# Kernel optimization log

Measured on AMD Instinct MI355X. Metric: run time of the kernel, lower is better.

Reference implementation:

```python
import jax, jax.numpy as jnp
import numpy as np

N_NODES = 50000
N_EDGES = 800000
D = 128


def setup_inputs() -> dict:
    key = jax.random.key(0)
    ks = jax.random.split(key, 8)
    x = jax.random.normal(ks[0], (N_NODES, D), dtype=jnp.float32)
    src = jax.random.randint(ks[1], (N_EDGES,), 0, N_NODES, dtype=jnp.int64)
    dst = jax.random.randint(ks[2], (N_EDGES,), 0, N_NODES, dtype=jnp.int64)
    edge_weights = jax.random.uniform(ks[3], (N_EDGES,), dtype=jnp.float32)
    scale = 1.0 / np.sqrt(D)
    W1 = jax.random.normal(ks[4], (D, D), dtype=jnp.float32) * scale
    b1 = jnp.zeros((D,), dtype=jnp.float32)
    W2 = jax.random.normal(ks[5], (D, D), dtype=jnp.float32) * scale
    b2 = jnp.zeros((D,), dtype=jnp.float32)
    return {"x": x, "src": src, "dst": dst, "edge_weights": edge_weights,
            "W1": W1, "b1": b1, "W2": W2, "b2": b2}


def reference(x, src, dst, edge_weights, W1, b1, W2, b2):
    n_nodes = x.shape[0]
    # out-degrees (edges where node is the source), clamped to >= 1
    deg = jax.ops.segment_sum(jnp.ones_like(src, dtype=x.dtype), src,
                              num_segments=n_nodes)
    deg = jnp.maximum(deg, 1.0)
    # per-edge symmetric-normalization coefficient: 1/sqrt(deg_u * deg_v)
    coef = jax.lax.rsqrt(deg[src] * deg[dst]) * edge_weights  # [E]
    # gather-multiply-scatter: sum_{u->v} x[u] * coef into node v
    msgs = x[src] * coef[:, None]                              # [E, D]
    agg = jax.ops.segment_sum(msgs, dst, num_segments=n_nodes)  # [N, D]
    # FFN: Linear -> ReLU -> Linear (dropout = 0)
    h = jax.nn.relu(agg @ W1 + b1)
    return h @ W2 + b2
```

## Files before the change

kernel.cpp:

```cpp
#include <hip/hip_runtime.h>

#define NN 50000
#define NE 800000
#define D  128
#define HB 128
#define CH 6272
#define PW 50176
#define XB 128
#define RB2 98
#define GRANGE 12544

typedef short short8 __attribute__((ext_vector_type(8)));
typedef float f32x4  __attribute__((ext_vector_type(4)));
typedef unsigned char u8;

__device__ __forceinline__ ushort f2bf(float f) {
    union { float f; unsigned u; } v; v.f = f;
    unsigned r = v.u + 0x7FFFu + ((v.u >> 16) & 1u);
    return (ushort)(r >> 16);
}


__global__ __launch_bounds__(1024) void prep_kernel(const int* __restrict__ src,
                                                    const int* __restrict__ dst,
                                                    const float* __restrict__ x,
                                                    const float* __restrict__ W1,
                                                    const float* __restrict__ W2,
                                                    u8* __restrict__ psrc,
                                                    u8* __restrict__ pdst,
                                                    ushort* __restrict__ xbf,
                                                    ushort* __restrict__ W1t,
                                                    ushort* __restrict__ W2t) {
    __shared__ unsigned bins[2 * PW / 4];
    const int t = threadIdx.x, b = blockIdx.x;

    if (b < HB) {
        for (int i = t; i < 2 * PW / 16; i += 1024)
            ((uint4*)bins)[i] = make_uint4(0, 0, 0, 0);
        __syncthreads();
        const int base = b * CH;
#pragma unroll
        for (int i = 0; i < 2; ++i) {
            int e0 = base + i * 4096 + t * 4;
            if (e0 < base + CH && e0 < NE) {
                int4 s4 = *(const int4*)(src + e0);
                int4 d4 = *(const int4*)(dst + e0);
                atomicAdd(&bins[s4.x >> 2], 1u << ((s4.x & 3) << 3));
                atomicAdd(&bins[s4.y >> 2], 1u << ((s4.y & 3) << 3));
                atomicAdd(&bins[s4.z >> 2], 1u << ((s4.z & 3) << 3));
                atomicAdd(&bins[s4.w >> 2], 1u << ((s4.w & 3) << 3));
                atomicAdd(&bins[PW / 4 + (d4.x >> 2)], 1u << ((d4.x & 3) << 3));
                atomicAdd(&bins[PW / 4 + (d4.y >> 2)], 1u << ((d4.y & 3) << 3));
                atomicAdd(&bins[PW / 4 + (d4.z >> 2)], 1u << ((d4.z & 3) << 3));
                atomicAdd(&bins[PW / 4 + (d4.w >> 2)], 1u << ((d4.w & 3) << 3));
            }
        }
        __syncthreads();
        uint4* os = (uint4*)(psrc + (size_t)b * PW);
        uint4* od = (uint4*)(pdst + (size_t)b * PW);
        for (int i = t; i < PW / 16; i += 1024) {
            os[i] = ((const uint4*)bins)[i];
            od[i] = ((const uint4*)(bins + PW / 4))[i];
        }
    } else if (b < HB + 4) {
        int c = (b - HB) * 1024 + t;
        if (c < 4096) {
            const float* W = (c < 2048) ? W1 : W2;
            ushort* Wt     = (c < 2048) ? W1t : W2t;
            int cc = c & 2047;
            int n  = cc >> 4;
            int k0 = (cc & 15) * 8;
            ushort tmp[8];
#pragma unroll
            for (int j = 0; j < 8; ++j) tmp[j] = f2bf(W[(k0 + j) * D + n]);
            *reinterpret_cast<uint4*>(Wt + n * D + k0) = *reinterpret_cast<uint4*>(tmp);
        }
    } else {
        for (int i = (b - HB - 4) * 1024 + t; i < NN * D / 8; i += XB * 1024) {
            const float4* p = (const float4*)(x + (size_t)i * 8);
            float4 v0 = p[0], v1 = p[1];
            ushort tmp[8];
            tmp[0] = f2bf(v0.x); tmp[1] = f2bf(v0.y); tmp[2] = f2bf(v0.z); tmp[3] = f2bf(v0.w);
            tmp[4] = f2bf(v1.x); tmp[5] = f2bf(v1.y); tmp[6] = f2bf(v1.z); tmp[7] = f2bf(v1.w);
            *reinterpret_cast<uint4*>(xbf + (size_t)i * 8) = *reinterpret_cast<uint4*>(tmp);
        }
    }
}

__global__ __launch_bounds__(256) void xprep_kernel(const float* __restrict__ x,
                                                    ushort* __restrict__ xbf) {
    int i = blockIdx.x * 256 + threadIdx.x;
    if (i >= NN * D / 8) return;
    const float4* p = (const float4*)(x + (size_t)i * 8);
    float4 v0 = p[0], v1 = p[1];
    ushort tmp[8];
    tmp[0] = f2bf(v0.x); tmp[1] = f2bf(v0.y); tmp[2] = f2bf(v0.z); tmp[3] = f2bf(v0.w);
    tmp[4] = f2bf(v1.x); tmp[5] = f2bf(v1.y); tmp[6] = f2bf(v1.z); tmp[7] = f2bf(v1.w);
    *reinterpret_cast<uint4*>(xbf + (size_t)i * 8) = *reinterpret_cast<uint4*>(tmp);
}


__global__ __launch_bounds__(1024) void reduce_kernel(const unsigned* __restrict__ psrc32,
                                                      unsigned* __restrict__ pdst32,
                                                      float* __restrict__ rsq,
                                                      int* __restrict__ cnt,
                                                      int* __restrict__ bsum98) {
    __shared__ int sm[128];
    const int t = threadIdx.x;
    const int g = (blockIdx.x * 1024 + t) >> 3;
    const int c = t & 7;
    const size_t stride = PW / 4;

    unsigned wv[16];
#pragma unroll
    for (int i = 0; i < 16; ++i)
        wv[i] = pdst32[(size_t)(c * 16 + i) * stride + g];
    unsigned t02 = 0, t13 = 0;
#pragma unroll
    for (int i = 0; i < 16; ++i) {
        t02 += wv[i] & 0x00FF00FFu;
        t13 += (wv[i] >> 8) & 0x00FF00FFu;
    }
    unsigned p02 = 0, p13 = 0;
#pragma unroll
    for (int i = 0; i < 16; ++i) {
        unsigned w = psrc32[(size_t)(c * 16 + i) * stride + g];
        p02 += w & 0x00FF00FFu;
        p13 += (w >> 8) & 0x00FF00FFu;
    }
    unsigned i02 = t02, i13 = t13;
#pragma unroll
    for (int off = 1; off < 8; off <<= 1) {
        unsigned v02 = __shfl_up(i02, off, 8);
        unsigned v13 = __shfl_up(i13, off, 8);
        if (c >= off) { i02 += v02; i13 += v13; }
    }
    unsigned q02 = p02, q13 = p13, u02 = t02, u13 = t13;
#pragma unroll
    for (int off = 1; off < 8; off <<= 1) {
        q02 += __shfl_xor(q02, off, 8);
        q13 += __shfl_xor(q13, off, 8);
        u02 += __shfl_xor(u02, off, 8);
        u13 += __shfl_xor(u13, off, 8);
    }
    unsigned r02 = i02 - t02, r13 = i13 - t13;
#pragma unroll
    for (int i = 0; i < 16; ++i) {
        unsigned w = wv[i];
        pdst32[(size_t)(c * 16 + i) * stride + g] =
            (r02 & 0xFFu) | ((r13 & 0xFFu) << 8) |
            (r02 & 0x00FF0000u) | ((r13 & 0x00FF0000u) << 8);
        r02 += w & 0x00FF00FFu;
        r13 += (w >> 8) & 0x00FF00FFu;
    }
    int tct = 0;
    if (c == 0) {
        int v0 = g * 4;
        int dg_[4] = { (int)(q02 & 0xFFFFu), (int)(q13 & 0xFFFFu),
                       (int)(q02 >> 16),     (int)(q13 >> 16) };
        int ct_[4] = { (int)(u02 & 0xFFFFu), (int)(u13 & 0xFFFFu),
                       (int)(u02 >> 16),     (int)(u13 >> 16) };
        tct = ct_[0] + ct_[1] + ct_[2] + ct_[3];
        if (v0 + 3 < NN) {
            *(float4*)(rsq + v0) = make_float4(rsqrtf(fmaxf((float)dg_[0], 1.f)),
                                               rsqrtf(fmaxf((float)dg_[1], 1.f)),
                                               rsqrtf(fmaxf((float)dg_[2], 1.f)),
                                               rsqrtf(fmaxf((float)dg_[3], 1.f)));
            *(int4*)(cnt + v0) = make_int4(ct_[0], ct_[1], ct_[2], ct_[3]);
        } else {
            for (int j = 0; j < 4; ++j)
                if (v0 + j < NN) {
                    rsq[v0 + j] = rsqrtf(fmaxf((float)dg_[j], 1.f));
                    cnt[v0 + j] = ct_[j];
                }
        }
        sm[t >> 3] = tct;
    }
    __syncthreads();
    for (int s = 64; s > 0; s >>= 1) {
        if (t < s) sm[t] += sm[t + s];
        __syncthreads();
    }
    if (t == 0) bsum98[blockIdx.x] = sm[0];
}


__global__ __launch_bounds__(512) void scan_write(const int* __restrict__ cnt,
                                                  const int* __restrict__ bsum98,
                                                  int* __restrict__ offs) {
    __shared__ int sm[512];
    const int b = blockIdx.x, t = threadIdx.x;
    sm[t] = (t < RB2 && t < b) ? bsum98[t] : 0;
    __syncthreads();
    for (int s = 256; s > 0; s >>= 1) {
        if (t < s) sm[t] += sm[t + s];
        __syncthreads();
    }
    int base = sm[0];
    __syncthreads();
    int i = b * 512 + t;
    int v = (i < NN) ? cnt[i] : 0;
    sm[t] = v;
    __syncthreads();
    for (int d2 = 1; d2 < 512; d2 <<= 1) {
        int u = (t >= d2) ? sm[t - d2] : 0;
        __syncthreads();
        sm[t] += u;
        __syncthreads();
    }
    if (i < NN) offs[i] = base + sm[t] - v;
    if (b == 0 && t == 0) offs[NN] = NE;
}


__global__ __launch_bounds__(1024) void scatter_kernel(const int* __restrict__ src,
                                                       const int* __restrict__ dst,
                                                       const float* __restrict__ ew,
                                                       const float* __restrict__ rsq,
                                                       const int* __restrict__ offs,
                                                       const u8* __restrict__ pd,
                                                       unsigned* __restrict__ csr) {
    __shared__ unsigned cur[PW / 4];
    const int t = threadIdx.x, b = blockIdx.x;
    for (int i = t; i < PW / 16; i += 1024)
        ((uint4*)cur)[i] = make_uint4(0, 0, 0, 0);
    __syncthreads();

    const u8* pdrow = pd + (size_t)b * PW;
    const int base = b * CH;
#pragma unroll
    for (int i = 0; i < 2; ++i) {
        int e0 = base + i * 4096 + t * 4;
        if (e0 < base + CH && e0 < NE) {
            int4 s4 = *(const int4*)(src + e0);
            int4 d4 = *(const int4*)(dst + e0);
            float4 w4 = *(const float4*)(ew + e0);
#pragma unroll
            for (int j = 0; j < 4; ++j) {
                int s = (j == 0) ? s4.x : (j == 1) ? s4.y : (j == 2) ? s4.z : s4.w;
                int d = (j == 0) ? d4.x : (j == 1) ? d4.y : (j == 2) ? d4.z : d4.w;
                float w = (j == 0) ? w4.x : (j == 1) ? w4.y : (j == 2) ? w4.z : w4.w;
                int sh = (d & 3) << 3;
                unsigned old = atomicAdd(&cur[d >> 2], 1u << sh);
                int rel = (int)((old >> sh) & 0xFFu);
                int pos = offs[d] + (int)pdrow[d] + rel;
                float coef = rsq[s] * rsq[d] * w;
                csr[pos] = (unsigned)s | ((unsigned)f2bf(coef) << 16);
            }
        }
    }
}


__global__ __launch_bounds__(256) void gather_bf16_kernel(const int* __restrict__ offs,
                                                          const unsigned* __restrict__ csr,
                                                          const ushort* __restrict__ xbf,
                                                          float* __restrict__ agg) {
    int v = blockIdx.x * 8 + (threadIdx.x >> 5);
    if (v >= NN) return;
    const int lane = threadIdx.x & 31;
    const int half = (threadIdx.x >> 5) & 1;
    const int beg = offs[v], end = offs[v + 1];
    float a0 = 0.f, a1 = 0.f, a2 = 0.f, a3 = 0.f;
#pragma unroll
    for (int p = 0; p < 4; ++p) {
        const unsigned lo = p * GRANGE;
        for (int i0 = beg; i0 < end; i0 += 32) {
            int n = end - i0; if (n > 32) n = 32;
            unsigned ej = (lane < n) ? csr[i0 + lane] : 0u;
            bool inr = (lane < n) && ((unsigned)(ej & 0xFFFFu) - lo < (unsigned)GRANGE);
            unsigned m = (unsigned)(__ballot(inr) >> (half * 32));
            while (m) {
                int j = __builtin_ctz(m); m &= m - 1;
                unsigned e = __shfl(ej, j, 32);
                float c = __int_as_float(e & 0xFFFF0000u);
                uint2 u = ((const uint2*)(xbf + (size_t)(e & 0xFFFFu) * D))[lane];
                a0 = fmaf(__int_as_float((int)(u.x << 16)),         c, a0);
                a1 = fmaf(__int_as_float((int)(u.x & 0xFFFF0000u)), c, a1);
                a2 = fmaf(__int_as_float((int)(u.y << 16)),         c, a2);
                a3 = fmaf(__int_as_float((int)(u.y & 0xFFFF0000u)), c, a3);
            }
        }
    }
    ((float4*)(agg + (size_t)v * D))[lane] = make_float4(a0, a1, a2, a3);
}


__global__ __launch_bounds__(256) void ffn_mfma_kernel(const float* __restrict__ agg,
                                                       const ushort* __restrict__ W1t,
                                                       const ushort* __restrict__ W2t,
                                                       const float* __restrict__ b1,
                                                       const float* __restrict__ b2,
                                                       float* __restrict__ out) {
    __shared__ ushort Wt[128 * 128];
    __shared__ ushort hS[4][16 * 128];

    const int t  = threadIdx.x;
    const int w  = t >> 6;
    const int l  = t & 63;
    const int lr = l & 15;
    const int lk = l >> 4;
    const int r0 = blockIdx.x * 64;

    for (int i = 0; i < 8; ++i) {
        int c = i * 256 + t;
        int n = c >> 4;
        int slot = c & 15;
        uint4 v = ((const uint4*)W1t)[c];
        int byte = n * 256 + ((slot * 16) ^ ((n & 7) << 4));
        *(uint4*)((char*)Wt + byte) = v;
    }

    const int arow = r0 + w * 16 + lr;
    short8 afrag[4];
#pragma unroll
    for (int kb = 0; kb < 4; ++kb) {
        int k = kb * 32 + lk * 8;
        float4 v0 = make_float4(0.f, 0.f, 0.f, 0.f), v1 = v0;
        if (arow < NN) {
            const float4* ap = (const float4*)(agg + (size_t)arow * D + k);
            v0 = ap[0]; v1 = ap[1];
        }
        short8 a;
        a[0] = (short)f2bf(v0.x); a[1] = (short)f2bf(v0.y);
        a[2] = (short)f2bf(v0.z); a[3] = (short)f2bf(v0.w);
        a[4] = (short)f2bf(v1.x); a[5] = (short)f2bf(v1.y);
        a[6] = (short)f2bf(v1.z); a[7] = (short)f2bf(v1.w);
        afrag[kb] = a;
    }
    __syncthreads();

    f32x4 acc[8];
#pragma unroll
    for (int nt = 0; nt < 8; ++nt) acc[nt] = (f32x4){0.f, 0.f, 0.f, 0.f};
#pragma unroll
    for (int kb = 0; kb < 4; ++kb) {
        int kbyte = (kb * 32 + lk * 8) * 2;
#pragma unroll
        for (int nt = 0; nt < 8; ++nt) {
            int n = nt * 16 + lr;
            short8 b = *(const short8*)((const char*)Wt + n * 256 + (kbyte ^ ((n & 7) << 4)));
            acc[nt] = __builtin_amdgcn_mfma_f32_16x16x32_bf16(afrag[kb], b, acc[nt], 0, 0, 0);
        }
    }
#pragma unroll
    for (int nt = 0; nt < 8; ++nt) {
        int col = nt * 16 + lr;
        float bb = b1[col];
#pragma unroll
        for (int r = 0; r < 4; ++r) {
            int row = lk * 4 + r;
            float h = fmaxf(acc[nt][r] + bb, 0.0f);
            int byte = row * 256 + ((col * 2) ^ ((row & 7) << 4));
            *(ushort*)((char*)&hS[w][0] + byte) = f2bf(h);
        }
    }
    __syncthreads();

    for (int i = 0; i < 8; ++i) {
        int c = i * 256 + t;
        int n = c >> 4;
        int slot = c & 15;
        uint4 v = ((const uint4*)W2t)[c];
        int byte = n * 256 + ((slot * 16) ^ ((n & 7) << 4));
        *(uint4*)((char*)Wt + byte) = v;
    }
    __syncthreads();

    short8 hfrag[4];
#pragma unroll
    for (int kb = 0; kb < 4; ++kb) {
        int kbyte = (kb * 32 + lk * 8) * 2;
        hfrag[kb] = *(const short8*)((const char*)&hS[w][0] + lr * 256 + (kbyte ^ ((lr & 7) << 4)));
    }
#pragma unroll
    for (int nt = 0; nt < 8; ++nt) acc[nt] = (f32x4){0.f, 0.f, 0.f, 0.f};
#pragma unroll
    for (int kb = 0; kb < 4; ++kb) {
        int kbyte = (kb * 32 + lk * 8) * 2;
#pragma unroll
        for (int nt = 0; nt < 8; ++nt) {
            int n = nt * 16 + lr;
            short8 b = *(const short8*)((const char*)Wt + n * 256 + (kbyte ^ ((n & 7) << 4)));
            acc[nt] = __builtin_amdgcn_mfma_f32_16x16x32_bf16(hfrag[kb], b, acc[nt], 0, 0, 0);
        }
    }
#pragma unroll
    for (int nt = 0; nt < 8; ++nt) {
        int col = nt * 16 + lr;
        float bb = b2[col];
#pragma unroll
        for (int r = 0; r < 4; ++r) {
            int row = r0 + w * 16 + lk * 4 + r;
            if (row < NN) out[(size_t)row * D + col] = acc[nt][r] + bb;
        }
    }
}


extern "C" void kernel_launch(void* const* d_in, const int* in_sizes, int n_in,
                              void* d_out, int out_size, void* d_ws, size_t ws_size,
                              hipStream_t stream) {
    const float* x  = (const float*)d_in[0];
    const int* src  = (const int*)d_in[1];
    const int* dst  = (const int*)d_in[2];
    const float* ew = (const float*)d_in[3];
    const float* W1 = (const float*)d_in[4];
    const float* b1 = (const float*)d_in[5];
    const float* W2 = (const float*)d_in[6];
    const float* b2 = (const float*)d_in[7];
    float* out = (float*)d_out;

    char* base = (char*)d_ws;
    size_t off = 0;
    auto alloc = [&](size_t bytes) { char* p = base + off; off = (off + bytes + 15) & ~(size_t)15; return p; };
    u8* psrc      = (u8*)alloc((size_t)HB * PW);
    u8* pdst      = (u8*)alloc((size_t)HB * PW);
    float* rsq    = (float*)alloc((size_t)NN * 4);
    int* cnt      = (int*)alloc((size_t)NN * 4);
    int* offs     = (int*)alloc((size_t)(NN + 1) * 4);
    int* bsum98   = (int*)alloc((size_t)RB2 * 4);
    unsigned* csr = (unsigned*)alloc((size_t)NE * 4);
    ushort* W1t   = (ushort*)alloc((size_t)D * D * 2);
    ushort* W2t   = (ushort*)alloc((size_t)D * D * 2);
    ushort* xbf_own = (ushort*)alloc((size_t)NN * D * 2);
    bool own_xbf = ws_size >= off;
    ushort* xbf = own_xbf ? xbf_own : (ushort*)psrc;

    int prep_grid = own_xbf ? (HB + 4 + XB) : (HB + 4);
    prep_kernel<<<prep_grid, 1024, 0, stream>>>(src, dst, x, W1, W2,
                                                psrc, pdst, xbf, W1t, W2t);
    reduce_kernel<<<RB2, 1024, 0, stream>>>((const unsigned*)psrc, (unsigned*)pdst,
                                            rsq, cnt, bsum98);
    scan_write<<<RB2, 512, 0, stream>>>(cnt, bsum98, offs);
    scatter_kernel<<<HB, 1024, 0, stream>>>(src, dst, ew, rsq, offs, pdst, csr);
    if (!own_xbf)
        xprep_kernel<<<(NN * D / 8 + 255) / 256, 256, 0, stream>>>(x, xbf);
    gather_bf16_kernel<<<(NN + 7) / 8, 256, 0, stream>>>(offs, csr, xbf, out);
    ffn_mfma_kernel<<<(NN + 63) / 64, 256, 0, stream>>>(out, W1t, W2t, b1, b2, out);
}
```

Baseline: 141.7 us.

## Fuse CSR gather into FFN kernel and unroll edge loads by four

The separate gather and FFN kernels become one kernel. Each 64-row block gathers its aggregated rows straight into shared memory as bf16 and then runs both MFMA layers, so the fp32 agg round-trip through global memory disappears. The old four-pass source-range filtering, which was meant to improve cache locality, is replaced by a single pass that issues four independent row loads per step for more memory-level parallelism. The cost is fewer, longer blocks, where load imbalance from uneven degrees can stall the whole block before the MFMA phase, and the gather loses its L2 locality partitioning.

Result: slower. 148.3 us (+4.7%).

```diff
diff --git a/kernel.cpp b/kernel.cpp
--- a/kernel.cpp
+++ b/kernel.cpp
@@ -8,7 +8,6 @@
 #define PW 50176
 #define XB 128
 #define RB2 98
-#define GRANGE 12544
 
 typedef short short8 __attribute__((ext_vector_type(8)));
 typedef float f32x4  __attribute__((ext_vector_type(4)));
@@ -153,14 +152,12 @@
         r02 += w & 0x00FF00FFu;
         r13 += (w >> 8) & 0x00FF00FFu;
     }
-    int tct = 0;
     if (c == 0) {
         int v0 = g * 4;
         int dg_[4] = { (int)(q02 & 0xFFFFu), (int)(q13 & 0xFFFFu),
                        (int)(q02 >> 16),     (int)(q13 >> 16) };
         int ct_[4] = { (int)(u02 & 0xFFFFu), (int)(u13 & 0xFFFFu),
                        (int)(u02 >> 16),     (int)(u13 >> 16) };
-        tct = ct_[0] + ct_[1] + ct_[2] + ct_[3];
         if (v0 + 3 < NN) {
             *(float4*)(rsq + v0) = make_float4(rsqrtf(fmaxf((float)dg_[0], 1.f)),
                                                rsqrtf(fmaxf((float)dg_[1], 1.f)),
@@ -174,7 +171,7 @@
                     cnt[v0 + j] = ct_[j];
                 }
         }
-        sm[t >> 3] = tct;
+        sm[t >> 3] = ct_[0] + ct_[1] + ct_[2] + ct_[3];
     }
     __syncthreads();
     for (int s = 64; s > 0; s >>= 1) {
@@ -252,84 +249,97 @@
 }
 
 
-__global__ __launch_bounds__(256) void gather_bf16_kernel(const int* __restrict__ offs,
-                                                          const unsigned* __restrict__ csr,
-                                                          const ushort* __restrict__ xbf,
-                                                          float* __restrict__ agg) {
-    int v = blockIdx.x * 8 + (threadIdx.x >> 5);
-    if (v >= NN) return;
-    const int lane = threadIdx.x & 31;
-    const int half = (threadIdx.x >> 5) & 1;
-    const int beg = offs[v], end = offs[v + 1];
-    float a0 = 0.f, a1 = 0.f, a2 = 0.f, a3 = 0.f;
-#pragma unroll
-    for (int p = 0; p < 4; ++p) {
-        const unsigned lo = p * GRANGE;
-        for (int i0 = beg; i0 < end; i0 += 32) {
-            int n = end - i0; if (n > 32) n = 32;
-            unsigned ej = (lane < n) ? csr[i0 + lane] : 0u;
-            bool inr = (lane < n) && ((unsigned)(ej & 0xFFFFu) - lo < (unsigned)GRANGE);
-            unsigned m = (unsigned)(__ballot(inr) >> (half * 32));
-            while (m) {
-                int j = __builtin_ctz(m); m &= m - 1;
-                unsigned e = __shfl(ej, j, 32);
-                float c = __int_as_float(e & 0xFFFF0000u);
-                uint2 u = ((const uint2*)(xbf + (size_t)(e & 0xFFFFu) * D))[lane];
-                a0 = fmaf(__int_as_float((int)(u.x << 16)),         c, a0);
-                a1 = fmaf(__int_as_float((int)(u.x & 0xFFFF0000u)), c, a1);
-                a2 = fmaf(__int_as_float((int)(u.y << 16)),         c, a2);
-                a3 = fmaf(__int_as_float((int)(u.y & 0xFFFF0000u)), c, a3);
-            }
-        }
-    }
-    ((float4*)(agg + (size_t)v * D))[lane] = make_float4(a0, a1, a2, a3);
-}
-
-
-__global__ __launch_bounds__(256) void ffn_mfma_kernel(const float* __restrict__ agg,
-                                                       const ushort* __restrict__ W1t,
-                                                       const ushort* __restrict__ W2t,
-                                                       const float* __restrict__ b1,
-                                                       const float* __restrict__ b2,
-                                                       float* __restrict__ out) {
+__global__ __launch_bounds__(256) void gather_ffn_kernel(const int* __restrict__ offs,
+                                                         const unsigned* __restrict__ csr,
+                                                         const ushort* __restrict__ xbf,
+                                                         const ushort* __restrict__ W1t,
+                                                         const ushort* __restrict__ W2t,
+                                                         const float* __restrict__ b1,
+                                                         const float* __restrict__ b2,
+                                                         float* __restrict__ out) {
     __shared__ ushort Wt[128 * 128];
-    __shared__ ushort hS[4][16 * 128];
+    __shared__ ushort aT[64 * 128];
 
     const int t  = threadIdx.x;
     const int w  = t >> 6;
     const int l  = t & 63;
     const int lr = l & 15;
     const int lk = l >> 4;
+    const int g  = t >> 5;
+    const int lane = t & 31;
     const int r0 = blockIdx.x * 64;
 
     for (int i = 0; i < 8; ++i) {
         int c = i * 256 + t;
-        int n = c >> 4;
-        int slot = c & 15;
+        int n = c >> 4, slot = c & 15;
         uint4 v = ((const uint4*)W1t)[c];
-        int byte = n * 256 + ((slot * 16) ^ ((n & 7) << 4));
-        *(uint4*)((char*)Wt + byte) = v;
-    }
-
-    const int arow = r0 + w * 16 + lr;
+        *(uint4*)((char*)Wt + n * 256 + ((slot * 16) ^ ((n & 7) << 4))) = v;
+    }
+
+    for (int i = 0; i < 8; ++i) {
+        int rr = g * 8 + i;
+        int v = r0 + rr;
+        float a0 = 0.f, a1 = 0.f, a2 = 0.f, a3 = 0.f;
+        if (v < NN) {
+            int beg = offs[v], end = offs[v + 1];
+            for (int i0 = beg; i0 < end; i0 += 32) {
+                int n = end - i0; if (n > 32) n = 32;
+                unsigned ej = (lane < n) ? csr[i0 + lane] : 0u;
+                int j = 0;
+                for (; j + 3 < n; j += 4) {
+                    unsigned e0 = __shfl(ej, j,     32);
+                    unsigned e1 = __shfl(ej, j + 1, 32);
+                    unsigned e2 = __shfl(ej, j + 2, 32);
+                    unsigned e3 = __shfl(ej, j + 3, 32);
+                    uint2 u0 = ((const uint2*)(xbf + (size_t)(e0 & 0xFFFFu) * D))[lane];
+                    uint2 u1 = ((const uint2*)(xbf + (size_t)(e1 & 0xFFFFu) * D))[lane];
+                    uint2 u2 = ((const uint2*)(xbf + (size_t)(e2 & 0xFFFFu) * D))[lane];
+                    uint2 u3 = ((const uint2*)(xbf + (size_t)(e3 & 0xFFFFu) * D))[lane];
+                    float c0 = __int_as_float(e0 & 0xFFFF0000u);
+                    float c1 = __int_as_float(e1 & 0xFFFF0000u);
+                    float c2 = __int_as_float(e2 & 0xFFFF0000u);
+                    float c3 = __int_as_float(e3 & 0xFFFF0000u);
+                    a0 = fmaf(__int_as_float((int)(u0.x << 16)),         c0, a0);
+                    a1 = fmaf(__int_as_float((int)(u0.x & 0xFFFF0000u)), c0, a1);
+                    a2 = fmaf(__int_as_float((int)(u0.y << 16)),         c0, a2);
+                    a3 = fmaf(__int_as_float((int)(u0.y & 0xFFFF0000u)), c0, a3);
+                    a0 = fmaf(__int_as_float((int)(u1.x << 16)),         c1, a0);
+                    a1 = fmaf(__int_as_float((int)(u1.x & 0xFFFF0000u)), c1, a1);
+                    a2 = fmaf(__int_as_float((int)(u1.y << 16)),         c1, a2);
+                    a3 = fmaf(__int_as_float((int)(u1.y & 0xFFFF0000u)), c1, a3);
+                    a0 = fmaf(__int_as_float((int)(u2.x << 16)),         c2, a0);
+                    a1 = fmaf(__int_as_float((int)(u2.x & 0xFFFF0000u)), c2, a1);
+                    a2 = fmaf(__int_as_float((int)(u2.y << 16)),         c2, a2);
+                    a3 = fmaf(__int_as_float((int)(u2.y & 0xFFFF0000u)), c2, a3);
+                    a0 = fmaf(__int_as_float((int)(u3.x << 16)),         c3, a0);
+                    a1 = fmaf(__int_as_float((int)(u3.x & 0xFFFF0000u)), c3, a1);
+                    a2 = fmaf(__int_as_float((int)(u3.y << 16)),         c3, a2);
+                    a3 = fmaf(__int_as_float((int)(u3.y & 0xFFFF0000u)), c3, a3);
+                }
+                for (; j < n; ++j) {
+                    unsigned e = __shfl(ej, j, 32);
+                    float c = __int_as_float(e & 0xFFFF0000u);
+                    uint2 u = ((const uint2*)(xbf + (size_t)(e & 0xFFFFu) * D))[lane];
+                    a0 = fmaf(__int_as_float((int)(u.x << 16)),         c, a0);
+                    a1 = fmaf(__int_as_float((int)(u.x & 0xFFFF0000u)), c, a1);
+                    a2 = fmaf(__int_as_float((int)(u.y << 16)),         c, a2);
+                    a3 = fmaf(__int_as_float((int)(u.y & 0xFFFF0000u)), c, a3);
+                }
+            }
+        }
+        unsigned lo = (unsigned)f2bf(a0) | ((unsigned)f2bf(a1) << 16);
+        unsigned hi = (unsigned)f2bf(a2) | ((unsigned)f2bf(a3) << 16);
+        *(uint2*)((char*)aT + rr * 256 + ((lane * 8) ^ ((rr & 7) << 4))) = make_uint2(lo, hi);
+    }
+    __syncthreads();
+
+    const int arow_l = w * 16 + lr;
     short8 afrag[4];
 #pragma unroll
     for (int kb = 0; kb < 4; ++kb) {
-        int k = kb * 32 + lk * 8;
-        float4 v0 = make_float4(0.f, 0.f, 0.f, 0.f), v1 = v0;
-        if (arow < NN) {
-            const float4* ap = (const float4*)(agg + (size_t)arow * D + k);
-            v0 = ap[0]; v1 = ap[1];
-        }
-        short8 a;
-        a[0] = (short)f2bf(v0.x); a[1] = (short)f2bf(v0.y);
-        a[2] = (short)f2bf(v0.z); a[3] = (short)f2bf(v0.w);
-        a[4] = (short)f2bf(v1.x); a[5] = (short)f2bf(v1.y);
-        a[6] = (short)f2bf(v1.z); a[7] = (short)f2bf(v1.w);
-        afrag[kb] = a;
-    }
-    __syncthreads();
-
+        int kbyte = (kb * 32 + lk * 8) * 2;
+        afrag[kb] = *(const short8*)((const char*)aT + arow_l * 256 + (kbyte ^ ((arow_l & 7) << 4)));
+    }
     f32x4 acc[8];
 #pragma unroll
     for (int nt = 0; nt < 8; ++nt) acc[nt] = (f32x4){0.f, 0.f, 0.f, 0.f};
@@ -349,21 +359,18 @@
         float bb = b1[col];
 #pragma unroll
         for (int r = 0; r < 4; ++r) {
-            int row = lk * 4 + r;
+            int row = w * 16 + lk * 4 + r;
             float h = fmaxf(acc[nt][r] + bb, 0.0f);
-            int byte = row * 256 + ((col * 2) ^ ((row & 7) << 4));
-            *(ushort*)((char*)&hS[w][0] + byte) = f2bf(h);
+            *(ushort*)((char*)aT + row * 256 + ((col * 2) ^ ((row & 7) << 4))) = f2bf(h);
         }
     }
     __syncthreads();
 
     for (int i = 0; i < 8; ++i) {
         int c = i * 256 + t;
-        int n = c >> 4;
-        int slot = c & 15;
+        int n = c >> 4, slot = c & 15;
         uint4 v = ((const uint4*)W2t)[c];
-        int byte = n * 256 + ((slot * 16) ^ ((n & 7) << 4));
-        *(uint4*)((char*)Wt + byte) = v;
+        *(uint4*)((char*)Wt + n * 256 + ((slot * 16) ^ ((n & 7) << 4))) = v;
     }
     __syncthreads();
 
@@ -371,7 +378,7 @@
 #pragma unroll
     for (int kb = 0; kb < 4; ++kb) {
         int kbyte = (kb * 32 + lk * 8) * 2;
-        hfrag[kb] = *(const short8*)((const char*)&hS[w][0] + lr * 256 + (kbyte ^ ((lr & 7) << 4)));
+        hfrag[kb] = *(const short8*)((const char*)aT + arow_l * 256 + (kbyte ^ ((arow_l & 7) << 4)));
     }
 #pragma unroll
     for (int nt = 0; nt < 8; ++nt) acc[nt] = (f32x4){0.f, 0.f, 0.f, 0.f};
@@ -436,6 +443,6 @@
     scatter_kernel<<<HB, 1024, 0, stream>>>(src, dst, ew, rsq, offs, pdst, csr);
     if (!own_xbf)
         xprep_kernel<<<(NN * D / 8 + 255) / 256, 256, 0, stream>>>(x, xbf);
-    gather_bf16_kernel<<<(NN + 7) / 8, 256, 0, stream>>>(offs, csr, xbf, out);
-    ffn_mfma_kernel<<<(NN + 63) / 64, 256, 0, stream>>>(out, W1t, W2t, b1, b2, out);
-}
+    gather_ffn_kernel<<<(NN + 63) / 64, 256, 0, stream>>>(offs, csr, xbf,
+                                                          W1t, W2t, b1, b2, out);
+}
```
